# Optimization experiments

Measured on AMD Instinct MI355X. Metric: run time of the kernel, lower is better.

## Reference

```python
import jax, jax.numpy as jnp
import numpy as np

P_DIM, L_DIM, D, O = 1100, 1024, 1024, 1024  # protein/label embed dims, latent, mlp width
B, NL = 16, 5000  # num_sequences, num_labels


def setup_inputs() -> dict:
    key = jax.random.key(0)
    ks = jax.random.split(key, 10)
    s = 0.02
    return {
        "sequence_embeddings": jax.random.normal(ks[0], (B, P_DIM), jnp.float32),
        "label_embeddings": jax.random.normal(ks[1], (NL, L_DIM), jnp.float32),
        "Wp": jax.random.normal(ks[2], (D, P_DIM), jnp.float32) * s,  # W_p (no bias)
        "Wl": jax.random.normal(ks[3], (D, L_DIM), jnp.float32) * s,  # W_l (no bias)
        "W1": jax.random.normal(ks[4], (O, 2 * D), jnp.float32) * s,  # Linear(2D -> O)
        "b1": jnp.zeros((O,), jnp.float32),
        "W2": jax.random.normal(ks[5], (O, O), jnp.float32) * s,      # Linear(O -> O)
        "b2": jnp.zeros((O,), jnp.float32),
        "W3": jax.random.normal(ks[6], (1, O), jnp.float32) * s,      # Linear(O -> 1)
        "b3": jnp.zeros((1,), jnp.float32),
    }


def reference(sequence_embeddings, label_embeddings, Wp, Wl, W1, b1, W2, b2, W3, b3):
    # Latent projections
    P_e = sequence_embeddings @ Wp.T           # [B, D]
    L_e = label_embeddings @ Wl.T              # [NL, D]
    # First MLP layer on concat([P_e, L_e]) over the cross join, computed by
    # splitting W1 into its P and L halves and broadcast-summing (same math as
    # cat + Linear, avoids materializing the [B*NL, 2D] concat).
    hp = P_e @ W1[:, :D].T                     # [B, O]
    hl = L_e @ W1[:, D:].T                     # [NL, O]
    h = jax.nn.relu(hp[:, None, :] + hl[None, :, :] + b1)   # [B, NL, O]
    h = jax.nn.relu(h @ W2.T + b2)             # [B, NL, O]
    logits = (h @ W3.T + b3)[..., 0]           # [B, NL]
    return logits
```

## Files before the change

kernel.cpp:

```cpp
#include <hip/hip_runtime.h>
#include <hip/hip_bf16.h>
#include <stdint.h>

typedef __bf16 bf16;
typedef __bf16 bf16x4 __attribute__((ext_vector_type(4)));
typedef __bf16 bf16x8 __attribute__((ext_vector_type(8)));
typedef float floatx4 __attribute__((ext_vector_type(4)));

#define B_SEQ 16
#define NLBL  5000
#define DLAT  1024
#define PDIM  1100
#define NROWS (B_SEQ * NLBL)

__device__ __forceinline__ void gload_lds16(const bf16* g, bf16* l) {
    __builtin_amdgcn_global_load_lds(
        (const __attribute__((address_space(1))) void*)g,
        (__attribute__((address_space(3))) void*)l, 16, 0, 0);
}

__device__ __forceinline__ bf16x8 cvt8(const float* s) {
    floatx4 a = *(const floatx4*)s;
    floatx4 b = *(const floatx4*)(s + 4);
    bf16x8 o;
    o[0] = (bf16)a.x; o[1] = (bf16)a.y; o[2] = (bf16)a.z; o[3] = (bf16)a.w;
    o[4] = (bf16)b.x; o[5] = (bf16)b.y; o[6] = (bf16)b.z; o[7] = (bf16)b.w;
    return o;
}

#define PSEG_M    256
#define PSEG_LAB  2756
#define PSEG_W2   3268
#define PSEG_PE   3524
#define PSEG_END  3837

__global__ __launch_bounds__(256)
void prep_kernel(const float* __restrict__ label, bf16* __restrict__ label_b,
                 const float* __restrict__ W2, bf16* __restrict__ W2_b,
                 const float* __restrict__ W1, const float* __restrict__ Wl,
                 bf16* __restrict__ M_bf,
                 const float* __restrict__ seq, const float* __restrict__ Wp,
                 float* __restrict__ Pe,
                 float* __restrict__ out, const float* __restrict__ b3) {
    __shared__ bf16 MAs[64 * 72];
    __shared__ bf16 MBs[64 * 72];
    const int blk = blockIdx.x;
    const int t = threadIdx.x;

    if (blk < PSEG_M) {
        const int m0 = (blk >> 4) * 64;
        const int n0g = (blk & 15) * 64;
        const int wave = t >> 6, lane = t & 63;
        const int wm = (wave & 1) * 32, wn = (wave >> 1) * 32;
        const int lm = lane & 15, quad = lane >> 4;
        const int a_r = t >> 2, a_c = (t & 3) * 16;
        const int b_kr = t >> 4, b_l = (t & 15) * 4;
        floatx4 acc[2][2] = {};

        for (int k0 = 0; k0 < 1024; k0 += 64) {
            const float* ap = W1 + (size_t)(m0 + a_r) * 2048 + 1024 + k0 + a_c;
            *(bf16x8*)(MAs + a_r * 72 + a_c) = cvt8(ap);
            *(bf16x8*)(MAs + a_r * 72 + a_c + 8) = cvt8(ap + 8);
#pragma unroll
            for (int ps = 0; ps < 4; ++ps) {
                int kr = b_kr + ps * 16;
                floatx4 v = *(const floatx4*)(Wl + (size_t)(k0 + kr) * 1024 + n0g + b_l);
                MBs[(b_l + 0) * 72 + kr] = (bf16)v.x;
                MBs[(b_l + 1) * 72 + kr] = (bf16)v.y;
                MBs[(b_l + 2) * 72 + kr] = (bf16)v.z;
                MBs[(b_l + 3) * 72 + kr] = (bf16)v.w;
            }
            __syncthreads();
#pragma unroll
            for (int ks = 0; ks < 2; ++ks) {
                bf16x8 af[2], bg[2];
#pragma unroll
                for (int mi = 0; mi < 2; ++mi)
                    af[mi] = *(const bf16x8*)(MAs + (wm + mi * 16 + lm) * 72 + ks * 32 + quad * 8);
#pragma unroll
                for (int ni = 0; ni < 2; ++ni)
                    bg[ni] = *(const bf16x8*)(MBs + (wn + ni * 16 + lm) * 72 + ks * 32 + quad * 8);
#pragma unroll
                for (int mi = 0; mi < 2; ++mi)
#pragma unroll
                    for (int ni = 0; ni < 2; ++ni)
                        acc[mi][ni] = __builtin_amdgcn_mfma_f32_16x16x32_bf16(af[mi], bg[ni], acc[mi][ni], 0, 0, 0);
            }
            __syncthreads();
        }
#pragma unroll
        for (int mi = 0; mi < 2; ++mi)
#pragma unroll
            for (int r = 0; r < 4; ++r)
#pragma unroll
                for (int ni = 0; ni < 2; ++ni)
                    M_bf[(size_t)(m0 + wm + mi * 16 + quad * 4 + r) * 1024 + n0g + wn + ni * 16 + lm] =
                        (bf16)acc[mi][ni][r];
    } else if (blk < PSEG_LAB) {
        int i = (blk - PSEG_M) * 256 + t;
        ((bf16x8*)label_b)[i] = cvt8(label + (size_t)i * 8);
    } else if (blk < PSEG_W2) {
        int i = (blk - PSEG_LAB) * 256 + t;
        ((bf16x8*)W2_b)[i] = cvt8(W2 + (size_t)i * 8);
    } else if (blk < PSEG_PE) {
        int w = (blk - PSEG_W2) * 4 + (t >> 6);
        int l = t & 63;
        floatx4 wv[5];
#pragma unroll
        for (int k = 0; k < 5; ++k) {
            int g = l + 64 * k;
            wv[k] = (g < 275) ? *(const floatx4*)(Wp + (size_t)w * PDIM + g * 4)
                              : floatx4{0.f, 0.f, 0.f, 0.f};
        }
        for (int b = 0; b < B_SEQ; ++b) {
            float acc = 0.f;
#pragma unroll
            for (int k = 0; k < 5; ++k) {
                int g = l + 64 * k;
                if (g < 275) {
                    floatx4 sv = *(const floatx4*)(seq + (size_t)b * PDIM + g * 4);
                    acc += wv[k].x * sv.x + wv[k].y * sv.y + wv[k].z * sv.z + wv[k].w * sv.w;
                }
            }
#pragma unroll
            for (int off = 32; off; off >>= 1) acc += __shfl_xor(acc, off, 64);
            if (l == 0) Pe[b * DLAT + w] = acc;
        }
    } else {
        int i = (blk - PSEG_PE) * 256 + t;
        if (i < NROWS) out[i] = b3[0];
    }
}


__global__ __launch_bounds__(256)
void hpb_kernel(const float* __restrict__ Pe, const float* __restrict__ W1,
                const float* __restrict__ b1, float* __restrict__ hpb) {
    int w = blockIdx.x * 4 + (threadIdx.x >> 6);
    int l = threadIdx.x & 63;
    floatx4 wv[4];
#pragma unroll
    for (int k = 0; k < 4; ++k)
        wv[k] = *(const floatx4*)(W1 + (size_t)w * 2048 + (l + 64 * k) * 4);
    for (int b = 0; b < B_SEQ; ++b) {
        float acc = 0.f;
#pragma unroll
        for (int k = 0; k < 4; ++k) {
            floatx4 pv = *(const floatx4*)(Pe + (size_t)b * DLAT + (l + 64 * k) * 4);
            acc += wv[k].x * pv.x + wv[k].y * pv.y + wv[k].z * pv.z + wv[k].w * pv.w;
        }
#pragma unroll
        for (int off = 32; off; off >>= 1) acc += __shfl_xor(acc, off, 64);
        if (l == 0) hpb[b * DLAT + w] = acc + b1[w];
    }
}


__global__ __launch_bounds__(256)
void hl_h1_kernel(const bf16* __restrict__ A, const bf16* __restrict__ Bt,
                  const float* __restrict__ hpb, bf16* __restrict__ h1) {
    __shared__ __align__(16) char smem[25600];
    bf16* As = (bf16*)smem;
    bf16* Bs = (bf16*)(smem + 8192);
    bf16* Ls = (bf16*)smem;
    float* hpbs = (float*)(smem + 17408);

    const int t = threadIdx.x;
    const int d0 = blockIdx.x * 128;
    const int n0 = blockIdx.y * 64;
    const int wave = t >> 6, lane = t & 63;
    const int wm = (wave & 1) * 32;
    const int wn = (wave >> 1) * 64;
    const int lm = lane & 15, quad = lane >> 4;
    const int sw = lm & 7;
    const int srow = t >> 3;
    const int scg0 = t & 7;
    const int sbase = (t & 192) * 8;

    floatx4 acc[2][4] = {};

    for (int k0 = 0; k0 < 1024; k0 += 64) {
#pragma unroll
        for (int p = 0; p < 2; ++p) {
            int row = p * 32 + srow;
            int cg = scg0 ^ (row & 7);
            int grow = n0 + row; if (grow >= NLBL) grow = NLBL - 1;
            gload_lds16(A + (size_t)grow * 1024 + k0 + cg * 8, As + p * 2048 + sbase);
        }
#pragma unroll
        for (int p = 0; p < 4; ++p) {
            int row = p * 32 + srow;
            int cg = scg0 ^ (row & 7);
            gload_lds16(Bt + (size_t)(d0 + row) * 1024 + k0 + cg * 8, Bs + p * 2048 + sbase);
        }
        __syncthreads();
#pragma unroll
        for (int k = 0; k < 64; k += 32) {
            bf16x8 af[2], bg[4];
            int ko = (((k >> 3) + quad) ^ sw) * 8;
#pragma unroll
            for (int mi = 0; mi < 2; ++mi)
                af[mi] = *(const bf16x8*)(As + (wm + mi * 16 + lm) * 64 + ko);
#pragma unroll
            for (int ni = 0; ni < 4; ++ni)
                bg[ni] = *(const bf16x8*)(Bs + (wn + ni * 16 + lm) * 64 + ko);
#pragma unroll
            for (int mi = 0; mi < 2; ++mi)
#pragma unroll
                for (int ni = 0; ni < 4; ++ni)
                    acc[mi][ni] = __builtin_amdgcn_mfma_f32_16x16x32_bf16(af[mi], bg[ni], acc[mi][ni], 0, 0, 0);
        }
        __syncthreads();
    }

#pragma unroll
    for (int mi = 0; mi < 2; ++mi)
#pragma unroll
        for (int r = 0; r < 4; ++r)
#pragma unroll
            for (int ni = 0; ni < 4; ++ni)
                Ls[(wm + mi * 16 + quad * 4 + r) * 136 + wn + ni * 16 + lm] =
                    (bf16)acc[mi][ni][r];
    {
        int dl = (t & 31) * 4;
        int b = t >> 5;
        *(floatx4*)(hpbs + b * 128 + dl) =
            *(const floatx4*)(hpb + (size_t)b * DLAT + d0 + dl);
        *(floatx4*)(hpbs + (b + 8) * 128 + dl) =
            *(const floatx4*)(hpb + (size_t)(b + 8) * DLAT + d0 + dl);
    }
    __syncthreads();

    const int g = t & 15;
    const int r0 = t >> 4;
    bf16x8 hlv[4];
#pragma unroll
    for (int p = 0; p < 4; ++p)
        hlv[p] = *(const bf16x8*)(Ls + (p * 16 + r0) * 136 + g * 8);

    for (int b = 0; b < B_SEQ; ++b) {
        floatx4 h0 = *(const floatx4*)(hpbs + b * 128 + g * 8);
        floatx4 h4 = *(const floatx4*)(hpbs + b * 128 + g * 8 + 4);
        size_t rowbase = (size_t)b * NLBL * 1024;
#pragma unroll
        for (int p = 0; p < 4; ++p) {
            int n = n0 + p * 16 + r0;
            if (n >= NLBL) continue;
            bf16x8 o;
            o[0] = (bf16)fmaxf((float)hlv[p][0] + h0.x, 0.f);
            o[1] = (bf16)fmaxf((float)hlv[p][1] + h0.y, 0.f);
            o[2] = (bf16)fmaxf((float)hlv[p][2] + h0.z, 0.f);
            o[3] = (bf16)fmaxf((float)hlv[p][3] + h0.w, 0.f);
            o[4] = (bf16)fmaxf((float)hlv[p][4] + h4.x, 0.f);
            o[5] = (bf16)fmaxf((float)hlv[p][5] + h4.y, 0.f);
            o[6] = (bf16)fmaxf((float)hlv[p][6] + h4.z, 0.f);
            o[7] = (bf16)fmaxf((float)hlv[p][7] + h4.w, 0.f);
            *(bf16x8*)(h1 + rowbase + (size_t)n * 1024 + d0 + g * 8) = o;
        }
    }
}


__global__ __launch_bounds__(256)
void gemm_h2(const bf16* __restrict__ h1, const bf16* __restrict__ W2b,
             const float* __restrict__ b2, const float* __restrict__ W3,
             float* __restrict__ out) {
    __shared__ bf16 As[128 * 64];
    __shared__ bf16 Bs[128 * 64];
    const int t = threadIdx.x;
    int flat = blockIdx.x;
    int x = flat & 7;
    int s = flat >> 3;
    int mt, nt;
    if (s < 624) { mt = x * 78 + (s >> 3); nt = s & 7; }
    else         { mt = 624; nt = x; }
    const int m0 = mt * 128, n0 = nt * 128;

    const int wave = t >> 6, lane = t & 63;
    const int wm = (wave & 1) * 64, wn = (wave >> 1) * 64;
    const int lm = lane & 15, quad = lane >> 4;
    const int sw = lm & 7;
    const int srow = t >> 3;
    const int scg0 = t & 7;
    const int sbase = (t & 192) * 8;

    floatx4 acc[4][4] = {};
    const bf16* Abase = h1 + (size_t)m0 * 1024;
    const bf16* Bbase = W2b + (size_t)n0 * 1024;

    for (int k0 = 0; k0 < 1024; k0 += 64) {
#pragma unroll
        for (int p = 0; p < 4; ++p) {
            int row = p * 32 + srow;
            int cg = scg0 ^ (row & 7);
            gload_lds16(Abase + (size_t)row * 1024 + k0 + cg * 8, As + p * 2048 + sbase);
        }
#pragma unroll
        for (int p = 0; p < 4; ++p) {
            int row = p * 32 + srow;
            int cg = scg0 ^ (row & 7);
            gload_lds16(Bbase + (size_t)row * 1024 + k0 + cg * 8, Bs + p * 2048 + sbase);
        }
        __syncthreads();
#pragma unroll
        for (int k = 0; k < 64; k += 32) {
            bf16x8 af[4], bg[4];
            int ko = (((k >> 3) + quad) ^ sw) * 8;
#pragma unroll
            for (int mi = 0; mi < 4; ++mi)
                af[mi] = *(const bf16x8*)(As + (wm + mi * 16 + lm) * 64 + ko);
#pragma unroll
            for (int ni = 0; ni < 4; ++ni)
                bg[ni] = *(const bf16x8*)(Bs + (wn + ni * 16 + lm) * 64 + ko);
#pragma unroll
            for (int mi = 0; mi < 4; ++mi)
#pragma unroll
                for (int ni = 0; ni < 4; ++ni)
                    acc[mi][ni] = __builtin_amdgcn_mfma_f32_16x16x32_bf16(af[mi], bg[ni], acc[mi][ni], 0, 0, 0);
        }
        __syncthreads();
    }

    float w3v[4], b2v[4];
#pragma unroll
    for (int ni = 0; ni < 4; ++ni) {
        int col = n0 + wn + ni * 16 + lm;
        w3v[ni] = W3[col];
        b2v[ni] = b2[col];
    }
#pragma unroll
    for (int mi = 0; mi < 4; ++mi) {
#pragma unroll
        for (int r = 0; r < 4; ++r) {
            float sacc = 0.f;
#pragma unroll
            for (int ni = 0; ni < 4; ++ni)
                sacc += fmaxf(acc[mi][ni][r] + b2v[ni], 0.f) * w3v[ni];
            sacc += __shfl_xor(sacc, 1, 64);
            sacc += __shfl_xor(sacc, 2, 64);
            sacc += __shfl_xor(sacc, 4, 64);
            sacc += __shfl_xor(sacc, 8, 64);
            if (lm == 0)
                atomicAdd(out + m0 + wm + mi * 16 + quad * 4 + r, sacc);
        }
    }
}


extern "C" void kernel_launch(void* const* d_in, const int* in_sizes, int n_in,
                              void* d_out, int out_size, void* d_ws, size_t ws_size,
                              hipStream_t stream) {
    const float* seq   = (const float*)d_in[0];
    const float* label = (const float*)d_in[1];
    const float* Wp    = (const float*)d_in[2];
    const float* Wl    = (const float*)d_in[3];
    const float* W1    = (const float*)d_in[4];
    const float* b1    = (const float*)d_in[5];
    const float* W2    = (const float*)d_in[6];
    const float* b2    = (const float*)d_in[7];
    const float* W3    = (const float*)d_in[8];
    const float* b3    = (const float*)d_in[9];
    float* out = (float*)d_out;
    (void)n_in; (void)in_sizes; (void)out_size; (void)ws_size;

    size_t off = 0;
    auto alloc = [&](size_t bytes) {
        void* p = (char*)d_ws + off;
        off += (bytes + 255) & ~(size_t)255;
        return p;
    };
    bf16* label_b = (bf16*)alloc((size_t)NLBL * 1024 * 2);
    bf16* W2_b    = (bf16*)alloc((size_t)1024 * 1024 * 2);
    bf16* M_bf    = (bf16*)alloc((size_t)1024 * 1024 * 2);
    float* Pe     = (float*)alloc((size_t)B_SEQ * 1024 * 4);
    float* hpb    = (float*)alloc((size_t)B_SEQ * 1024 * 4);
    bf16* h1      = (bf16*)alloc((size_t)NROWS * 1024 * 2);

    prep_kernel<<<PSEG_END, 256, 0, stream>>>(label, label_b, W2, W2_b, W1, Wl,
                                              M_bf, seq, Wp, Pe, out, b3);
    hpb_kernel<<<256, 256, 0, stream>>>(Pe, W1, b1, hpb);
    hl_h1_kernel<<<dim3(8, 79), 256, 0, stream>>>(label_b, M_bf, hpb, h1);
    gemm_h2<<<5000, 256, 0, stream>>>(h1, W2_b, b2, W3, out);
}
```

Measured before the change: 333.2 us.

## Rewrite h2 GEMM as 256x256 tile, 8-wave double-buffered pipeline

Replaces the 128x128 single-buffered h2 GEMM with 256x256 tiles run by 512 threads (8 waves). The LDS is double-buffered so global-to-LDS prefetch of the next K-slice overlaps the MFMA work, and the MFMA phases are interleaved with barriers and s_setprio. This cuts global traffic per FLOP and hides load latency. The cost is 128 KB of LDS and more registers per block, which lowers occupancy, plus a clamp on out-of-range rows for the last partial M tile.

```diff
diff --git a/kernel.cpp b/kernel.cpp
--- a/kernel.cpp
+++ b/kernel.cpp
@@ -26,6 +26,12 @@
     o[0] = (bf16)a.x; o[1] = (bf16)a.y; o[2] = (bf16)a.z; o[3] = (bf16)a.w;
     o[4] = (bf16)b.x; o[5] = (bf16)b.y; o[6] = (bf16)b.z; o[7] = (bf16)b.w;
     return o;
+}
+
+__device__ __forceinline__ void barx() {
+    asm volatile("" ::: "memory");
+    __builtin_amdgcn_s_barrier();
+    asm volatile("" ::: "memory");
 }
 
 #define PSEG_M    256
@@ -261,75 +267,152 @@
 }
 
 
-__global__ __launch_bounds__(256)
+__device__ __forceinline__ void stage_A256(const bf16* __restrict__ src, bf16* dst,
+                                           int m0, int kc, int t) {
+#pragma unroll
+    for (int i = 0; i < 4; ++i) {
+        int s = t + i * 512;
+        int row = s >> 3;
+        int cg = (s & 7) ^ (row & 7);
+        int grow = m0 + row;
+        if (grow >= NROWS) grow = NROWS - 1;
+        gload_lds16(src + (size_t)grow * 1024 + kc + cg * 8, dst + s * 8);
+    }
+}
+
+__device__ __forceinline__ void stage_B256(const bf16* __restrict__ src, bf16* dst,
+                                           int n0, int kc, int t) {
+#pragma unroll
+    for (int i = 0; i < 4; ++i) {
+        int s = t + i * 512;
+        int row = s >> 3;
+        int cg = (s & 7) ^ (row & 7);
+        gload_lds16(src + (size_t)(n0 + row) * 1024 + kc + cg * 8, dst + s * 8);
+    }
+}
+
+__global__ __launch_bounds__(512, 2)
 void gemm_h2(const bf16* __restrict__ h1, const bf16* __restrict__ W2b,
              const float* __restrict__ b2, const float* __restrict__ W3,
              float* __restrict__ out) {
-    __shared__ bf16 As[128 * 64];
-    __shared__ bf16 Bs[128 * 64];
+    __shared__ bf16 As[32768];
+    __shared__ bf16 Bs[32768];
     const int t = threadIdx.x;
-    int flat = blockIdx.x;
-    int x = flat & 7;
-    int s = flat >> 3;
-    int mt, nt;
-    if (s < 624) { mt = x * 78 + (s >> 3); nt = s & 7; }
-    else         { mt = 624; nt = x; }
-    const int m0 = mt * 128, n0 = nt * 128;
+
+    int orig = blockIdx.x;
+    int xcd = orig & 7, idx = orig >> 3;
+    int wg = (xcd < 4 ? xcd * 157 : 628 + (xcd - 4) * 156) + idx;
+    const int mt = wg >> 2, nt = wg & 3;
+    const int m0 = mt * 256, n0 = nt * 256;
 
     const int wave = t >> 6, lane = t & 63;
-    const int wm = (wave & 1) * 64, wn = (wave >> 1) * 64;
+    const int wr = wave >> 2, wc = wave & 3;
+    const int wrow = wr * 128, wcol = wc * 64;
     const int lm = lane & 15, quad = lane >> 4;
-    const int sw = lm & 7;
-    const int srow = t >> 3;
-    const int scg0 = t & 7;
-    const int sbase = (t & 192) * 8;
-
-    floatx4 acc[4][4] = {};
-    const bf16* Abase = h1 + (size_t)m0 * 1024;
-    const bf16* Bbase = W2b + (size_t)n0 * 1024;
-
-    for (int k0 = 0; k0 < 1024; k0 += 64) {
-#pragma unroll
-        for (int p = 0; p < 4; ++p) {
-            int row = p * 32 + srow;
-            int cg = scg0 ^ (row & 7);
-            gload_lds16(Abase + (size_t)row * 1024 + k0 + cg * 8, As + p * 2048 + sbase);
-        }
-#pragma unroll
-        for (int p = 0; p < 4; ++p) {
-            int row = p * 32 + srow;
-            int cg = scg0 ^ (row & 7);
-            gload_lds16(Bbase + (size_t)row * 1024 + k0 + cg * 8, Bs + p * 2048 + sbase);
-        }
-        __syncthreads();
-#pragma unroll
-        for (int k = 0; k < 64; k += 32) {
-            bf16x8 af[4], bg[4];
-            int ko = (((k >> 3) + quad) ^ sw) * 8;
-#pragma unroll
-            for (int mi = 0; mi < 4; ++mi)
-                af[mi] = *(const bf16x8*)(As + (wm + mi * 16 + lm) * 64 + ko);
-#pragma unroll
-            for (int ni = 0; ni < 4; ++ni)
-                bg[ni] = *(const bf16x8*)(Bs + (wn + ni * 16 + lm) * 64 + ko);
-#pragma unroll
-            for (int mi = 0; mi < 4; ++mi)
-#pragma unroll
-                for (int ni = 0; ni < 4; ++ni)
-                    acc[mi][ni] = __builtin_amdgcn_mfma_f32_16x16x32_bf16(af[mi], bg[ni], acc[mi][ni], 0, 0, 0);
-        }
-        __syncthreads();
+    const int swz = lm & 7;
+
+    floatx4 acc[8][4] = {};
+
+    stage_A256(h1, As, m0, 0, t);
+    stage_B256(W2b, Bs, n0, 0, t);
+    asm volatile("s_waitcnt vmcnt(0)" ::: "memory");
+    barx();
+
+    for (int kt = 0; kt < 16; ++kt) {
+        const int db = kt & 1;
+        const bf16* Ad = As + db * 16384;
+        const bf16* Bd = Bs + db * 16384;
+        bf16* An = As + (db ^ 1) * 16384;
+        bf16* Bn = Bs + (db ^ 1) * 16384;
+        const bool pf = (kt < 15);
+        const int kc = (kt + 1) * 64;
+
+        bf16x8 a[4][2], blo[2][2], bhi[2][2];
+
+#pragma unroll
+        for (int mi = 0; mi < 4; ++mi) {
+            const bf16* rp = Ad + (wrow + mi * 16 + lm) * 64;
+            a[mi][0] = *(const bf16x8*)(rp + ((quad ^ swz) << 3));
+            a[mi][1] = *(const bf16x8*)(rp + (((4 + quad) ^ swz) << 3));
+        }
+#pragma unroll
+        for (int ni = 0; ni < 2; ++ni) {
+            const bf16* rp = Bd + (wcol + ni * 16 + lm) * 64;
+            blo[ni][0] = *(const bf16x8*)(rp + ((quad ^ swz) << 3));
+            blo[ni][1] = *(const bf16x8*)(rp + (((4 + quad) ^ swz) << 3));
+        }
+        if (pf) stage_A256(h1, An, m0, kc, t);
+        barx();
+        __builtin_amdgcn_s_setprio(1);
+#pragma unroll
+        for (int mi = 0; mi < 4; ++mi)
+#pragma unroll
+            for (int ni = 0; ni < 2; ++ni) {
+                acc[mi][ni] = __builtin_amdgcn_mfma_f32_16x16x32_bf16(a[mi][0], blo[ni][0], acc[mi][ni], 0, 0, 0);
+                acc[mi][ni] = __builtin_amdgcn_mfma_f32_16x16x32_bf16(a[mi][1], blo[ni][1], acc[mi][ni], 0, 0, 0);
+            }
+        __builtin_amdgcn_s_setprio(0);
+        barx();
+
+#pragma unroll
+        for (int ni = 0; ni < 2; ++ni) {
+            const bf16* rp = Bd + (wcol + 32 + ni * 16 + lm) * 64;
+            bhi[ni][0] = *(const bf16x8*)(rp + ((quad ^ swz) << 3));
+            bhi[ni][1] = *(const bf16x8*)(rp + (((4 + quad) ^ swz) << 3));
+        }
+        if (pf) stage_B256(W2b, Bn, n0, kc, t);
+        barx();
+        __builtin_amdgcn_s_setprio(1);
+#pragma unroll
+        for (int mi = 0; mi < 4; ++mi)
+#pragma unroll
+            for (int ni = 0; ni < 2; ++ni) {
+                acc[mi][2 + ni] = __builtin_amdgcn_mfma_f32_16x16x32_bf16(a[mi][0], bhi[ni][0], acc[mi][2 + ni], 0, 0, 0);
+                acc[mi][2 + ni] = __builtin_amdgcn_mfma_f32_16x16x32_bf16(a[mi][1], bhi[ni][1], acc[mi][2 + ni], 0, 0, 0);
+            }
+        __builtin_amdgcn_s_setprio(0);
+        barx();
+
+#pragma unroll
+        for (int mi = 0; mi < 4; ++mi) {
+            const bf16* rp = Ad + (wrow + 64 + mi * 16 + lm) * 64;
+            a[mi][0] = *(const bf16x8*)(rp + ((quad ^ swz) << 3));
+            a[mi][1] = *(const bf16x8*)(rp + (((4 + quad) ^ swz) << 3));
+        }
+        barx();
+        __builtin_amdgcn_s_setprio(1);
+#pragma unroll
+        for (int mi = 0; mi < 4; ++mi)
+#pragma unroll
+            for (int ni = 0; ni < 2; ++ni) {
+                acc[4 + mi][2 + ni] = __builtin_amdgcn_mfma_f32_16x16x32_bf16(a[mi][0], bhi[ni][0], acc[4 + mi][2 + ni], 0, 0, 0);
+                acc[4 + mi][2 + ni] = __builtin_amdgcn_mfma_f32_16x16x32_bf16(a[mi][1], bhi[ni][1], acc[4 + mi][2 + ni], 0, 0, 0);
+            }
+        __builtin_amdgcn_s_setprio(0);
+        barx();
+
+        __builtin_amdgcn_s_setprio(1);
+#pragma unroll
+        for (int mi = 0; mi < 4; ++mi)
+#pragma unroll
+            for (int ni = 0; ni < 2; ++ni) {
+                acc[4 + mi][ni] = __builtin_amdgcn_mfma_f32_16x16x32_bf16(a[mi][0], blo[ni][0], acc[4 + mi][ni], 0, 0, 0);
+                acc[4 + mi][ni] = __builtin_amdgcn_mfma_f32_16x16x32_bf16(a[mi][1], blo[ni][1], acc[4 + mi][ni], 0, 0, 0);
+            }
+        __builtin_amdgcn_s_setprio(0);
+        asm volatile("s_waitcnt vmcnt(0)" ::: "memory");
+        barx();
     }
 
     float w3v[4], b2v[4];
 #pragma unroll
     for (int ni = 0; ni < 4; ++ni) {
-        int col = n0 + wn + ni * 16 + lm;
+        int col = n0 + wcol + ni * 16 + lm;
         w3v[ni] = W3[col];
         b2v[ni] = b2[col];
     }
 #pragma unroll
-    for (int mi = 0; mi < 4; ++mi) {
+    for (int mi = 0; mi < 8; ++mi) {
 #pragma unroll
         for (int r = 0; r < 4; ++r) {
             float sacc = 0.f;
@@ -340,8 +423,9 @@
             sacc += __shfl_xor(sacc, 2, 64);
             sacc += __shfl_xor(sacc, 4, 64);
             sacc += __shfl_xor(sacc, 8, 64);
-            if (lm == 0)
-                atomicAdd(out + m0 + wm + mi * 16 + quad * 4 + r, sacc);
+            int row = m0 + wrow + mi * 16 + quad * 4 + r;
+            if (lm == 0 && row < NROWS)
+                atomicAdd(out + row, sacc);
         }
     }
 }
@@ -380,5 +464,5 @@
                                               M_bf, seq, Wp, Pe, out, b3);
     hpb_kernel<<<256, 256, 0, stream>>>(Pe, W1, b1, hpb);
     hl_h1_kernel<<<dim3(8, 79), 256, 0, stream>>>(label_b, M_bf, hpb, h1);
-    gemm_h2<<<5000, 256, 0, stream>>>(h1, W2_b, b2, W3, out);
-}
+    gemm_h2<<<1252, 512, 0, stream>>>(h1, W2_b, b2, W3, out);
+}
```

New measurement: 325.8 us. 2.2% less time.
